# Kernel optimization log

Hardware: AMD Instinct MI355X
Metric: run time of the kernel (lower is better)

Reference implementation:

```python
import jax, jax.numpy as jnp
import numpy as np

NEG_SLOPE = 0.2

def setup_inputs() -> dict:
    key = jax.random.key(0)
    k1, k2, k3, k4 = jax.random.split(key, 4)
    B, n, d_in, d_out = 8, 2048, 128, 128
    x = jax.random.normal(k1, (B, n, d_in), dtype=jnp.float32)
    adj = jax.random.uniform(k2, (B, n, n), dtype=jnp.float32)
    # glorot init for W: std = sqrt(2/(fan_in+fan_out))
    W = jax.random.normal(k3, (d_in, d_out), dtype=jnp.float32) * np.sqrt(2.0 / (d_in + d_out))
    a = jax.random.normal(k4, (2 * d_out,), dtype=jnp.float32) * np.sqrt(2.0 / (2 * d_out + 1))
    return {"x": x, "adj": adj, "W": W, "a": a}

def reference(x, adj, W, a):
    d_out = W.shape[1]
    h = jnp.einsum('bni,io->bno', x, W)               # [B,n,d_out]
    x_weighted = jnp.einsum('bnm,bmo->bno', adj, h)   # adj @ Wx
    # additive attention: a @ concat(h_i, h_j) == h_i@a_src + h_j@a_dst
    a_src, a_dst = a[:d_out], a[d_out:]
    s_i = h @ a_src                                   # [B,n]
    s_j = h @ a_dst                                   # [B,n]
    e = jax.nn.leaky_relu(s_i[:, :, None] + s_j[:, None, :], NEG_SLOPE)  # [B,n,n]
    alpha = jax.nn.softmax(e, axis=2)
    out = jnp.einsum('bnm,bmo->bno', alpha, h) + x_weighted
    return jax.nn.leaky_relu(out, NEG_SLOPE)
```

## Files before the change

### kernel.cpp

```cpp
#include <hip/hip_runtime.h>
#include <hip/hip_bf16.h>

#define NEG 0.2f
#define LOG2E 1.4426950408889634f

typedef __attribute__((ext_vector_type(8))) short bf16x8;
typedef __attribute__((ext_vector_type(4))) float f32x4;
typedef __attribute__((ext_vector_type(16))) float f32x16;
typedef __attribute__((ext_vector_type(4))) int int4v;

__device__ __forceinline__ float lrelu(float t){ return fmaxf(t, NEG * t); }
__device__ __forceinline__ float fast_exp2(float x){
  float r; asm("v_exp_f32 %0, %1" : "=v"(r) : "v"(x)); return r;
}
__device__ __forceinline__ unsigned short f2bf(float f){
  union { float f; unsigned int u; } v; v.f = f;
  unsigned int r = v.u + 0x7FFFu + ((v.u >> 16) & 1u);
  return (unsigned short)(r >> 16);
}

__global__ __launch_bounds__(256) void k0_wt(const float* __restrict__ W,
                                             unsigned short* __restrict__ Wt){
  __shared__ __align__(16) unsigned short wl[128*136];
  const int t = threadIdx.x;
  {
    const int k = t >> 1, oh = (t & 1) * 64;
#pragma unroll 8
    for (int e = 0; e < 64; ++e)
      wl[(oh + e)*136 + k] = f2bf(W[k*128 + oh + e]);
  }
  __syncthreads();
  {
    const int o = t >> 1, ks = (t & 1) * 64;
#pragma unroll
    for (int g = 0; g < 8; ++g){
      int4v v = *(const int4v*)(wl + o*136 + ks + g*8);
      *(int4v*)(Wt + o*128 + ks + g*8) = v;
    }
  }
}

__global__ __launch_bounds__(256) void k1_fused(const float* __restrict__ x,
                                                const unsigned short* __restrict__ Wt,
                                                const float* __restrict__ a,
                                                unsigned short* __restrict__ ht,
                                                float* __restrict__ ssrcL,
                                                float* __restrict__ sdstL){
  __shared__ __align__(16) unsigned short wtl[128*136];
  __shared__ __align__(16) unsigned short xl[32*136];
  __shared__ __align__(16) unsigned short tlw[128*34];
  __shared__ float sred[2][4][2][16];
  const int t = threadIdx.x;
  const int bx = blockIdx.x;
  const int b  = bx >> 6;
  const int jt = bx & 63;
  const long rowbase = (long)bx * 32;
  {
    const int o = t >> 1, seg = (t & 1) * 64;
    const int4v* src = (const int4v*)(Wt + o*128 + seg);
    int4v* dst = (int4v*)(wtl + o*136 + seg);
#pragma unroll
    for (int g = 0; g < 8; ++g) dst[g] = src[g];
  }
  {
    const int i = t >> 3, ks = (t & 7) * 16;
    const f32x4* src = (const f32x4*)(x + (rowbase + i)*128 + ks);
    unsigned int q[8];
#pragma unroll
    for (int g = 0; g < 4; ++g){
      f32x4 v = src[g];
      q[g*2]   = (unsigned)f2bf(v[0]) | ((unsigned)f2bf(v[1]) << 16);
      q[g*2+1] = (unsigned)f2bf(v[2]) | ((unsigned)f2bf(v[3]) << 16);
    }
    int4v* dst = (int4v*)(xl + i*136 + ks);
    dst[0] = *(int4v*)&q[0];
    dst[1] = *(int4v*)&q[4];
  }
  __syncthreads();
  const int w = t >> 6, lane = t & 63, lr = lane & 15, hi = lane >> 4;
  f32x4 zro = {0.f, 0.f, 0.f, 0.f};
  f32x4 acc00 = zro, acc01 = zro, acc10 = zro, acc11 = zro;
#pragma unroll
  for (int ks = 0; ks < 4; ++ks){
    const bf16x8 a0 = *(const bf16x8*)(wtl + (w*32      + lr)*136 + ks*32 + hi*8);
    const bf16x8 a1 = *(const bf16x8*)(wtl + (w*32 + 16 + lr)*136 + ks*32 + hi*8);
    const bf16x8 b0 = *(const bf16x8*)(xl + (     lr)*136 + ks*32 + hi*8);
    const bf16x8 b1 = *(const bf16x8*)(xl + (16 + lr)*136 + ks*32 + hi*8);
    acc00 = __builtin_amdgcn_mfma_f32_16x16x32_bf16(a0, b0, acc00, 0, 0, 0);
    acc01 = __builtin_amdgcn_mfma_f32_16x16x32_bf16(a0, b1, acc01, 0, 0, 0);
    acc10 = __builtin_amdgcn_mfma_f32_16x16x32_bf16(a1, b0, acc10, 0, 0, 0);
    acc11 = __builtin_amdgcn_mfma_f32_16x16x32_bf16(a1, b1, acc11, 0, 0, 0);
  }
  {
    const f32x4 as0 = *(const f32x4*)(a +       w*32      + hi*4);
    const f32x4 as1 = *(const f32x4*)(a +       w*32 + 16 + hi*4);
    const f32x4 ad0 = *(const f32x4*)(a + 128 + w*32      + hi*4);
    const f32x4 ad1 = *(const f32x4*)(a + 128 + w*32 + 16 + hi*4);
    float ps0, ps1, pd0, pd1;
    {
      f32x4 u = acc00*as0 + acc10*as1;  ps0 = u[0]+u[1]+u[2]+u[3];
      f32x4 v = acc01*as0 + acc11*as1;  ps1 = v[0]+v[1]+v[2]+v[3];
      f32x4 p = acc00*ad0 + acc10*ad1;  pd0 = p[0]+p[1]+p[2]+p[3];
      f32x4 r = acc01*ad0 + acc11*ad1;  pd1 = r[0]+r[1]+r[2]+r[3];
    }
#pragma unroll
    for (int off = 16; off <= 32; off <<= 1){
      ps0 += __shfl_xor(ps0, off); ps1 += __shfl_xor(ps1, off);
      pd0 += __shfl_xor(pd0, off); pd1 += __shfl_xor(pd1, off);
    }
    if (hi == 0){
      sred[0][w][0][lr] = ps0; sred[0][w][1][lr] = ps1;
      sred[1][w][0][lr] = pd0; sred[1][w][1][lr] = pd1;
    }
  }
#pragma unroll
  for (int q = 0; q < 4; ++q){
    tlw[(w*32      + hi*4 + q)*34      + lr] = f2bf(acc00[q]);
    tlw[(w*32      + hi*4 + q)*34 + 16 + lr] = f2bf(acc01[q]);
    tlw[(w*32 + 16 + hi*4 + q)*34      + lr] = f2bf(acc10[q]);
    tlw[(w*32 + 16 + hi*4 + q)*34 + 16 + lr] = f2bf(acc11[q]);
  }
  __syncthreads();
  {
    const int o = t >> 1, jseg = (t & 1) * 16;
    const unsigned int* src = (const unsigned int*)(tlw + o*34 + jseg);
    unsigned int p[8];
#pragma unroll
    for (int g = 0; g < 8; ++g) p[g] = src[g];
    unsigned short* dst = ht + (long)b*262144 + (long)o*2048 + jt*32 + jseg;
    ((int4v*)dst)[0] = *(int4v*)&p[0];
    ((int4v*)dst)[1] = *(int4v*)&p[4];
  }
  if (t < 64){
    const int sel = t >> 5, jl = t & 31;
    const int ig = jl >> 4, l2 = jl & 15;
    const float s = sred[sel][0][ig][l2] + sred[sel][1][ig][l2]
                  + sred[sel][2][ig][l2] + sred[sel][3][ig][l2];
    if (sel == 0) ssrcL[rowbase + jl] = s * LOG2E;
    else          sdstL[rowbase + jl] = s * LOG2E;
  }
}

__global__ __launch_bounds__(256) void k2_max(const float* __restrict__ sdstL,
                                              float* __restrict__ M){
  __shared__ float red[4];
  const int b = blockIdx.x, t = threadIdx.x;
  const int lane = t & 63, w = t >> 6;
  const f32x4* sd = (const f32x4*)(sdstL + (long)b*2048 + t*8);
  f32x4 v0 = sd[0], v1 = sd[1];
  float mx = fmaxf(fmaxf(fmaxf(v0[0], v0[1]), fmaxf(v0[2], v0[3])),
                   fmaxf(fmaxf(v1[0], v1[1]), fmaxf(v1[2], v1[3])));
#pragma unroll
  for (int off = 1; off <= 32; off <<= 1) mx = fmaxf(mx, __shfl_xor(mx, off));
  if (lane == 0) red[w] = mx;
  __syncthreads();
  if (t == 0) M[b] = fmaxf(fmaxf(red[0], red[1]), fmaxf(red[2], red[3]));
}

__global__ __launch_bounds__(256) void k2_ml(const float* __restrict__ ssrcL,
                                             const float* __restrict__ sdstL,
                                             const float* __restrict__ M,
                                             float* __restrict__ carr){
  const int lane = threadIdx.x & 63;
  const long row = (long)blockIdx.x * 4 + (threadIdx.x >> 6);
  const int b = (int)(row >> 11);
  const float siL = ssrcL[row];
  const float mL = lrelu(siL + M[b]);
  const float* sd = sdstL + (long)b*2048;
  float sum = 0.f;
#pragma unroll
  for (int k = 0; k < 8; ++k){
    f32x4 v = *(const f32x4*)(sd + lane*4 + k*256);
#pragma unroll
    for (int e = 0; e < 4; ++e) sum += fast_exp2(lrelu(siL + v[e]) - mL);
  }
#pragma unroll
  for (int off = 1; off <= 32; off <<= 1) sum += __shfl_xor(sum, off);
  if (lane == 0) carr[row] = mL + __log2f(sum);
}

__global__ __launch_bounds__(256, 2) void k3_main(const float* __restrict__ adj,
                                                  const unsigned short* __restrict__ ht,
                                                  const float* __restrict__ ssrcL,
                                                  const float* __restrict__ sdstL,
                                                  const float* __restrict__ carr,
                                                  float* __restrict__ out){
  __shared__ __align__(16) char smem[81920];
  unsigned short (*httile)[128][128] = (unsigned short (*)[128][128])smem;
  unsigned short (*wtile)[32][128]   = (unsigned short (*)[32][128])(smem + 65536);
  const int t    = threadIdx.x;
  const int bxr  = blockIdx.x;
  const int bx   = ((bxr & 7) << 6) | (bxr >> 3);
  const int b    = bx >> 6;
  const int i0   = (bx & 63) * 32;
  const int w    = t >> 6, lane = t & 63;
  const int r32  = lane & 31, hl = lane >> 5;
  const int xr   = r32 & 15;
  const int c0   = w*4 + hl*2;
  const long rowg = (long)b*2048 + i0 + r32;
  const float siL = ssrcL[rowg];
  const float Ci  = carr[rowg];
  const float* adjL = adj + rowg*2048 + w*32 + hl*16;
  const float* sdbL = sdstL + (long)b*2048 + w*32 + hl*16;
  const unsigned short* sgrow = ht + (long)b*262144 + (long)(w*32 + (lane >> 4))*2048;
  const int sch = (lane & 15) ^ (lane >> 4);

  f32x16 acc;
#pragma unroll
  for (int e = 0; e < 16; ++e) acc[e] = 0.f;
  f32x4 avA[4], dvA[4], avB[4], dvB[4];

#define K3_STAGE(B2, WIN) do{                                                    \
    _Pragma("unroll")                                                            \
    for (int ii = 0; ii < 8; ++ii){                                              \
      __builtin_amdgcn_global_load_lds(                                          \
        (const __attribute__((address_space(1))) void*)                          \
          (sgrow + (long)ii*8192 + (WIN) + (sch ^ ((ii*4) & 15))*8),             \
        (__attribute__((address_space(3))) void*)&httile[B2][w*32 + ii*4][0],    \
        16, 0, 0);                                                               \
    }                                                                            \
  }while(0)

#define K3_REFILL(AV, DV, WIN) do{                                               \
    _Pragma("unroll")                                                            \
    for (int g = 0; g < 4; ++g){                                                 \
      AV[g] = *(const f32x4*)(adjL + (WIN) + g*4);                               \
      DV[g] = *(const f32x4*)(sdbL + (WIN) + g*4);                               \
    }                                                                            \
  }while(0)

  K3_STAGE(0, 0);
  K3_REFILL(avA, dvA, 0);
  K3_REFILL(avB, dvB, 128);
  asm volatile("s_waitcnt vmcnt(16)" ::: "memory");
  __builtin_amdgcn_sched_barrier(0);

#define K3_STEP(KT, BUF, DO_STAGE, DO_REFILL, VMSTR, AV, DV) do{                 \
    if (DO_STAGE) K3_STAGE((BUF)^1, ((KT)+1)*128);                               \
    {  unsigned pw[8];                                                           \
       _Pragma("unroll")                                                         \
       for (int g = 0; g < 4; ++g){                                              \
         float w0 = AV[g][0] + fast_exp2(lrelu(siL + DV[g][0]) - Ci);            \
         float w1 = AV[g][1] + fast_exp2(lrelu(siL + DV[g][1]) - Ci);            \
         float w2 = AV[g][2] + fast_exp2(lrelu(siL + DV[g][2]) - Ci);            \
         float w3 = AV[g][3] + fast_exp2(lrelu(siL + DV[g][3]) - Ci);            \
         pw[g*2]   = __builtin_amdgcn_perm(__float_as_uint(w1), __float_as_uint(w0), 0x07060302u); \
         pw[g*2+1] = __builtin_amdgcn_perm(__float_as_uint(w3), __float_as_uint(w2), 0x07060302u); \
       }                                                                         \
       int4v iv0 = {(int)pw[0], (int)pw[1], (int)pw[2], (int)pw[3]};             \
       int4v iv1 = {(int)pw[4], (int)pw[5], (int)pw[6], (int)pw[7]};             \
       *(int4v*)&wtile[BUF][r32][( c0      ^ xr)*8] = iv0;                       \
       *(int4v*)&wtile[BUF][r32][((c0 + 1) ^ xr)*8] = iv1;                       \
    }                                                                            \
    if (DO_REFILL) K3_REFILL(AV, DV, ((KT)+2)*128);                              \
    asm volatile("s_waitcnt vmcnt(" VMSTR ") lgkmcnt(0)" ::: "memory");          \
    __builtin_amdgcn_sched_barrier(0);                                           \
    __builtin_amdgcn_s_barrier();                                                \
    __builtin_amdgcn_sched_barrier(0);                                           \
    __builtin_amdgcn_s_setprio(1);                                               \
    _Pragma("unroll")                                                            \
    for (int g = 0; g < 8; ++g){                                                 \
      const int cp = ((g*2 + hl) ^ xr)*8;                                        \
      const bf16x8 afr = *(const bf16x8*)&wtile[BUF][r32][cp];                   \
      const bf16x8 bfr = *(const bf16x8*)&httile[BUF][w*32 + r32][cp];           \
      acc = __builtin_amdgcn_mfma_f32_32x32x16_bf16(afr, bfr, acc, 0, 0, 0);     \
    }                                                                            \
    __builtin_amdgcn_s_setprio(0);                                               \
    __builtin_amdgcn_sched_barrier(0);                                           \
  }while(0)

  for (int kt = 0; kt < 14; kt += 2){
    K3_STEP(kt,     0, 1, 1, "16", avA, dvA);
    K3_STEP(kt + 1, 1, 1, 1, "16", avB, dvB);
  }
  K3_STEP(14, 0, 1, 0, "16", avA, dvA);
  K3_STEP(15, 1, 0, 0, "0",  avB, dvB);
#undef K3_STEP
#undef K3_STAGE
#undef K3_REFILL

#pragma unroll
  for (int rg = 0; rg < 16; ++rg){
    const int rr = (rg & 3) + 8*(rg >> 2) + 4*hl;
    out[((long)b*2048 + i0 + rr)*128 + w*32 + r32] = lrelu(acc[rg]);
  }
}

extern "C" void kernel_launch(void* const* d_in, const int* in_sizes, int n_in,
                              void* d_out, int out_size, void* d_ws, size_t ws_size,
                              hipStream_t stream){
  const float* x   = (const float*)d_in[0];
  const float* adj = (const float*)d_in[1];
  const float* W   = (const float*)d_in[2];
  const float* a   = (const float*)d_in[3];
  float* out = (float*)d_out;
  char* ws = (char*)d_ws;

  unsigned short* ht    = (unsigned short*)(ws);
  float*          ssrcL = (float*)(ws + 4194304);
  float*          sdstL = (float*)(ws + 4259840);
  float*          carr  = (float*)(ws + 4325376);
  unsigned short* Wt    = (unsigned short*)(ws + 4390912);
  float*          M     = (float*)(ws + 4423680);

  k0_wt   <<<1,    256, 0, stream>>>(W, Wt);
  k1_fused<<<512,  256, 0, stream>>>(x, Wt, a, ht, ssrcL, sdstL);
  k2_max  <<<8,    256, 0, stream>>>(sdstL, M);
  k2_ml   <<<4096, 256, 0, stream>>>(ssrcL, sdstL, M, carr);
  k3_main <<<512,  256, 0, stream>>>(adj, ht, ssrcL, sdstL, carr, out);
}
```

Measured before the change: 56.59 us.

## Halve K-tile to 64 and triple-buffer ht staging in main kernel

Cuts the main kernel's K tile from 128 to 64 columns and stages the transposed-h tiles through three LDS buffers with a prefetch distance of two, while keeping the weight tile double-buffered. The LDS swizzle is reworked to an 8-chunk XOR pattern for the narrower rows. The aim is to reduce LDS footprint and deepen the load pipeline so global loads overlap better with MFMA work. The trade-off is twice as many block barriers and iterations, each with fewer MFMAs to hide latency behind.

Result: slower. 59.29 us (+4.8%).

```diff
diff --git a/kernel.cpp b/kernel.cpp
--- a/kernel.cpp
+++ b/kernel.cpp
@@ -185,9 +185,9 @@
                                                   const float* __restrict__ sdstL,
                                                   const float* __restrict__ carr,
                                                   float* __restrict__ out){
-  __shared__ __align__(16) char smem[81920];
-  unsigned short (*httile)[128][128] = (unsigned short (*)[128][128])smem;
-  unsigned short (*wtile)[32][128]   = (unsigned short (*)[32][128])(smem + 65536);
+  __shared__ __align__(16) char smem[57344];
+  unsigned short (*httile)[128][64] = (unsigned short (*)[128][64])smem;
+  unsigned short (*wtile)[32][64]   = (unsigned short (*)[32][64])(smem + 49152);
   const int t    = threadIdx.x;
   const int bxr  = blockIdx.x;
   const int bx   = ((bxr & 7) << 6) | (bxr >> 3);
@@ -195,89 +195,91 @@
   const int i0   = (bx & 63) * 32;
   const int w    = t >> 6, lane = t & 63;
   const int r32  = lane & 31, hl = lane >> 5;
-  const int xr   = r32 & 15;
-  const int c0   = w*4 + hl*2;
+  const int r7v  = r32 & 7;
+  const int wchunk = (w*2 + hl) ^ r7v;
   const long rowg = (long)b*2048 + i0 + r32;
   const float siL = ssrcL[rowg];
   const float Ci  = carr[rowg];
-  const float* adjL = adj + rowg*2048 + w*32 + hl*16;
-  const float* sdbL = sdstL + (long)b*2048 + w*32 + hl*16;
-  const unsigned short* sgrow = ht + (long)b*262144 + (long)(w*32 + (lane >> 4))*2048;
-  const int sch = (lane & 15) ^ (lane >> 4);
+  const float* adjL = adj + rowg*2048 + w*16 + hl*8;
+  const float* sdbL = sdstL + (long)b*2048 + w*16 + hl*8;
+  const unsigned short* sgbase = ht + (long)b*262144
+                               + (long)(w*32 + (lane >> 3))*2048
+                               + ((lane & 7) ^ (lane >> 3)) * 8;
 
   f32x16 acc;
 #pragma unroll
   for (int e = 0; e < 16; ++e) acc[e] = 0.f;
-  f32x4 avA[4], dvA[4], avB[4], dvB[4];
-
-#define K3_STAGE(B2, WIN) do{                                                    \
+  f32x4 avA0, avA1, dvA0, dvA1, avB0, avB1, dvB0, dvB1;
+
+#define K3_STAGE(SB, WIN) do{                                                    \
     _Pragma("unroll")                                                            \
-    for (int ii = 0; ii < 8; ++ii){                                              \
+    for (int it = 0; it < 4; ++it)                                               \
       __builtin_amdgcn_global_load_lds(                                          \
-        (const __attribute__((address_space(1))) void*)                          \
-          (sgrow + (long)ii*8192 + (WIN) + (sch ^ ((ii*4) & 15))*8),             \
-        (__attribute__((address_space(3))) void*)&httile[B2][w*32 + ii*4][0],    \
-        16, 0, 0);                                                               \
+        (const __attribute__((address_space(1))) void*)(sgbase + (WIN) + it*16384), \
+        (__attribute__((address_space(3))) void*)&httile[SB][w*32 + it*8][0], 16, 0, 0); \
+  }while(0)
+
+#define K3_REFILL(AV0, AV1, DV0, DV1, WIN) do{                                   \
+    AV0 = *(const f32x4*)(adjL + (WIN));                                         \
+    AV1 = *(const f32x4*)(adjL + (WIN) + 4);                                     \
+    DV0 = *(const f32x4*)(sdbL + (WIN));                                         \
+    DV1 = *(const f32x4*)(sdbL + (WIN) + 4);                                     \
+  }while(0)
+
+#define K3_WEIGHTS(WB, AV0, AV1, DV0, DV1) do{                                   \
+    float wv[8];                                                                 \
+    _Pragma("unroll")                                                            \
+    for (int e = 0; e < 4; ++e){                                                 \
+      wv[e]   = AV0[e] + fast_exp2(lrelu(siL + DV0[e]) - Ci);                    \
+      wv[4+e] = AV1[e] + fast_exp2(lrelu(siL + DV1[e]) - Ci);                    \
     }                                                                            \
+    const unsigned p01 = __builtin_amdgcn_perm(__float_as_uint(wv[1]), __float_as_uint(wv[0]), 0x07060302u); \
+    const unsigned p23 = __builtin_amdgcn_perm(__float_as_uint(wv[3]), __float_as_uint(wv[2]), 0x07060302u); \
+    const unsigned p45 = __builtin_amdgcn_perm(__float_as_uint(wv[5]), __float_as_uint(wv[4]), 0x07060302u); \
+    const unsigned p67 = __builtin_amdgcn_perm(__float_as_uint(wv[7]), __float_as_uint(wv[6]), 0x07060302u); \
+    int4v ai = {(int)p01, (int)p23, (int)p45, (int)p67};                         \
+    *(int4v*)&wtile[WB][r32][wchunk*8] = ai;                                     \
   }while(0)
 
-#define K3_REFILL(AV, DV, WIN) do{                                               \
-    _Pragma("unroll")                                                            \
-    for (int g = 0; g < 4; ++g){                                                 \
-      AV[g] = *(const f32x4*)(adjL + (WIN) + g*4);                               \
-      DV[g] = *(const f32x4*)(sdbL + (WIN) + g*4);                               \
-    }                                                                            \
-  }while(0)
-
   K3_STAGE(0, 0);
-  K3_REFILL(avA, dvA, 0);
-  K3_REFILL(avB, dvB, 128);
-  asm volatile("s_waitcnt vmcnt(16)" ::: "memory");
+  K3_STAGE(1, 64);
+  K3_REFILL(avA0, avA1, dvA0, dvA1, 0);
+  K3_REFILL(avB0, avB1, dvB0, dvB1, 64);
+  asm volatile("s_waitcnt vmcnt(8)" ::: "memory");
   __builtin_amdgcn_sched_barrier(0);
 
-#define K3_STEP(KT, BUF, DO_STAGE, DO_REFILL, VMSTR, AV, DV) do{                 \
-    if (DO_STAGE) K3_STAGE((BUF)^1, ((KT)+1)*128);                               \
-    {  unsigned pw[8];                                                           \
-       _Pragma("unroll")                                                         \
-       for (int g = 0; g < 4; ++g){                                              \
-         float w0 = AV[g][0] + fast_exp2(lrelu(siL + DV[g][0]) - Ci);            \
-         float w1 = AV[g][1] + fast_exp2(lrelu(siL + DV[g][1]) - Ci);            \
-         float w2 = AV[g][2] + fast_exp2(lrelu(siL + DV[g][2]) - Ci);            \
-         float w3 = AV[g][3] + fast_exp2(lrelu(siL + DV[g][3]) - Ci);            \
-         pw[g*2]   = __builtin_amdgcn_perm(__float_as_uint(w1), __float_as_uint(w0), 0x07060302u); \
-         pw[g*2+1] = __builtin_amdgcn_perm(__float_as_uint(w3), __float_as_uint(w2), 0x07060302u); \
-       }                                                                         \
-       int4v iv0 = {(int)pw[0], (int)pw[1], (int)pw[2], (int)pw[3]};             \
-       int4v iv1 = {(int)pw[4], (int)pw[5], (int)pw[6], (int)pw[7]};             \
-       *(int4v*)&wtile[BUF][r32][( c0      ^ xr)*8] = iv0;                       \
-       *(int4v*)&wtile[BUF][r32][((c0 + 1) ^ xr)*8] = iv1;                       \
-    }                                                                            \
-    if (DO_REFILL) K3_REFILL(AV, DV, ((KT)+2)*128);                              \
-    asm volatile("s_waitcnt vmcnt(" VMSTR ") lgkmcnt(0)" ::: "memory");          \
-    __builtin_amdgcn_sched_barrier(0);                                           \
-    __builtin_amdgcn_s_barrier();                                                \
-    __builtin_amdgcn_sched_barrier(0);                                           \
-    __builtin_amdgcn_s_setprio(1);                                               \
-    _Pragma("unroll")                                                            \
-    for (int g = 0; g < 8; ++g){                                                 \
-      const int cp = ((g*2 + hl) ^ xr)*8;                                        \
-      const bf16x8 afr = *(const bf16x8*)&wtile[BUF][r32][cp];                   \
-      const bf16x8 bfr = *(const bf16x8*)&httile[BUF][w*32 + r32][cp];           \
-      acc = __builtin_amdgcn_mfma_f32_32x32x16_bf16(afr, bfr, acc, 0, 0, 0);     \
-    }                                                                            \
-    __builtin_amdgcn_s_setprio(0);                                               \
-    __builtin_amdgcn_sched_barrier(0);                                           \
-  }while(0)
-
-  for (int kt = 0; kt < 14; kt += 2){
-    K3_STEP(kt,     0, 1, 1, "16", avA, dvA);
-    K3_STEP(kt + 1, 1, 1, 1, "16", avB, dvB);
-  }
-  K3_STEP(14, 0, 1, 0, "16", avA, dvA);
-  K3_STEP(15, 1, 0, 0, "0",  avB, dvB);
-#undef K3_STEP
+#pragma unroll
+  for (int kt = 0; kt < 32; ++kt){
+    const int rb = kt % 3;
+    const int sb = (kt + 2) % 3;
+    const int wb = kt & 1;
+    if (kt < 30) K3_STAGE(sb, (kt + 2) * 64);
+    if (wb == 0) K3_WEIGHTS(0, avA0, avA1, dvA0, dvA1);
+    else         K3_WEIGHTS(1, avB0, avB1, dvB0, dvB1);
+    if (kt < 30){
+      if (wb == 0) K3_REFILL(avA0, avA1, dvA0, dvA1, (kt + 2) * 64);
+      else         K3_REFILL(avB0, avB1, dvB0, dvB1, (kt + 2) * 64);
+    }
+    if (kt < 30)       asm volatile("s_waitcnt vmcnt(16) lgkmcnt(0)" ::: "memory");
+    else if (kt == 30) asm volatile("s_waitcnt vmcnt(8) lgkmcnt(0)" ::: "memory");
+    else               asm volatile("s_waitcnt vmcnt(0) lgkmcnt(0)" ::: "memory");
+    __builtin_amdgcn_sched_barrier(0);
+    __builtin_amdgcn_s_barrier();
+    __builtin_amdgcn_sched_barrier(0);
+    __builtin_amdgcn_s_setprio(1);
+#pragma unroll
+    for (int g = 0; g < 4; ++g){
+      const int pos = ((2*g + hl) ^ r7v) * 8;
+      const bf16x8 afr = *(const bf16x8*)&wtile[wb][r32][pos];
+      const bf16x8 bfr = *(const bf16x8*)&httile[rb][w*32 + r32][pos];
+      acc = __builtin_amdgcn_mfma_f32_32x32x16_bf16(afr, bfr, acc, 0, 0, 0);
+    }
+    __builtin_amdgcn_s_setprio(0);
+    __builtin_amdgcn_sched_barrier(0);
+  }
 #undef K3_STAGE
 #undef K3_REFILL
+#undef K3_WEIGHTS
 
 #pragma unroll
   for (int rg = 0; rg < 16; ++rg){
```
